# Kernel tuning notes

Hardware: AMD Instinct MI355X
Metric: run time of the kernel (lower is better)

## Reference

```python
import jax, jax.numpy as jnp
import numpy as np

B, T, U, H = 16, 256, 96, 512


def setup_inputs() -> dict:
    key = jax.random.key(0)
    k1, k2, k3, k4 = jax.random.split(key, 4)
    f = jax.random.normal(k1, (B, T, H), dtype=jnp.float32)
    g = jax.random.normal(k2, (B, U, H), dtype=jnp.float32)
    f_len = jax.random.randint(k3, (B,), 1, T + 1, dtype=jnp.int32)
    g_len = jax.random.randint(k4, (B,), 1, U + 1, dtype=jnp.int32)
    return {"f": f, "g": g, "f_len": f_len, "g_len": g_len}


def reference(f, g, f_len, g_len):
    # f: (B, T, H), g: (B, U, H) -> h: (B, T, U, H)
    # h[b,t,u,:] = f[b,t,:] + g[b,u,:] for t < f_len[b], u < g_len[b]; else 0.
    Bc, Tc, Hc = f.shape
    Uc = g.shape[1]
    t_valid = jnp.arange(Tc)[None, :] < f_len[:, None]          # (B, T)
    u_valid = jnp.arange(Uc)[None, :] < g_len[:, None]          # (B, U)
    mask = (t_valid[:, :, None] & u_valid[:, None, :])[..., None]  # (B, T, U, 1)
    h = f[:, :, None, :] + g[:, None, :, :]                     # (B, T, U, H)
    return jnp.where(mask, h, jnp.zeros((), dtype=f.dtype))
```

## Files before the change

### kernel.cpp

```cpp
#include <hip/hip_runtime.h>
#include <hip/hip_bf16.h>


#define TJ_B 16
#define TJ_T 256
#define TJ_U 96
#define TJ_H 512
#define TJ_H4 (TJ_H / 4)

typedef float fx4 __attribute__((ext_vector_type(4)));

__global__ __launch_bounds__(256) void TransducerJoint_66915590472509_kernel(
    const fx4* __restrict__ f,
    const fx4* __restrict__ g,
    const int* __restrict__ f_len,
    const int* __restrict__ g_len,
    fx4* __restrict__ out)
{
    const int bt = blockIdx.x;
    const int b  = bt >> 8;
    const int t  = bt & 255;

    const int h4    = threadIdx.x & (TJ_H4 - 1);
    const int uhalf = threadIdx.x >> 7;

    const int flen = f_len[b];
    const int glen = g_len[b];
    const bool tvalid = (t < flen);

    fx4 fv = (fx4)0.f;
    if (tvalid) fv = f[(size_t)bt * TJ_H4 + h4];

    const fx4* gp = g + ((size_t)(b * TJ_U + uhalf)) * TJ_H4 + h4;
    fx4* op = out + ((size_t)bt * TJ_U + uhalf) * TJ_H4 + h4;

    #pragma unroll 8
    for (int u = uhalf; u < TJ_U; u += 2) {
        const fx4 gv = *gp;
        const bool ok = tvalid && (u < glen);
        fx4 r = ok ? (fv + gv) : (fx4)0.f;
        __builtin_nontemporal_store(r, op);
        gp += 2 * TJ_H4;
        op += 2 * TJ_H4;
    }
}

extern "C" void kernel_launch(void* const* d_in, const int* in_sizes, int n_in,
                              void* d_out, int out_size, void* d_ws, size_t ws_size,
                              hipStream_t stream) {
    const fx4* f     = (const fx4*)d_in[0];
    const fx4* g     = (const fx4*)d_in[1];
    const int* f_len = (const int*)d_in[2];
    const int* g_len = (const int*)d_in[3];
    fx4*       out   = (fx4*)d_out;

    const int nblocks = TJ_B * TJ_T;
    TransducerJoint_66915590472509_kernel<<<nblocks, 256, 0, stream>>>(
        f, g, f_len, g_len, out);
}
```

Measured before the change: 806.0 us.

## Process two time steps per block, keeping g slice in registers

Each block now handles two consecutive t values with 512 threads. Each thread loads its share of g[b] into 24 registers once and reuses it for both time steps, which halves g reads per output. The nontemporal stores are replaced with plain stores, and f is loaded unconditionally. The cost is more register pressure and half as many blocks.

```diff
diff --git a/kernel.cpp b/kernel.cpp
--- a/kernel.cpp
+++ b/kernel.cpp
@@ -5,43 +5,52 @@
 #define TJ_B 16
 #define TJ_T 256
 #define TJ_U 96
-#define TJ_H 512
-#define TJ_H4 (TJ_H / 4)
+#define TJ_H4 128
+#define TJ_TT 2
+#define TJ_NTH 512
+#define TJ_K ((TJ_U * TJ_H4) / TJ_NTH)
 
 typedef float fx4 __attribute__((ext_vector_type(4)));
 
-__global__ __launch_bounds__(256) void TransducerJoint_66915590472509_kernel(
+__global__ __launch_bounds__(TJ_NTH) void TransducerJoint_66915590472509_kernel(
     const fx4* __restrict__ f,
     const fx4* __restrict__ g,
     const int* __restrict__ f_len,
     const int* __restrict__ g_len,
     fx4* __restrict__ out)
 {
-    const int bt = blockIdx.x;
-    const int b  = bt >> 8;
-    const int t  = bt & 255;
-
-    const int h4    = threadIdx.x & (TJ_H4 - 1);
-    const int uhalf = threadIdx.x >> 7;
+    const int bid = blockIdx.x;
+    const int b   = bid >> 7;
+    const int t0  = (bid & 127) * TJ_TT;
+    const int i   = threadIdx.x;
+    const int h4  = i & (TJ_H4 - 1);
+    const int uu  = i >> 7;
 
     const int flen = f_len[b];
     const int glen = g_len[b];
-    const bool tvalid = (t < flen);
 
-    fx4 fv = (fx4)0.f;
-    if (tvalid) fv = f[(size_t)bt * TJ_H4 + h4];
+    fx4 fr[TJ_TT];
+    #pragma unroll
+    for (int tt = 0; tt < TJ_TT; ++tt)
+        fr[tt] = f[(size_t)(b * TJ_T + t0 + tt) * TJ_H4 + h4];
 
-    const fx4* gp = g + ((size_t)(b * TJ_U + uhalf)) * TJ_H4 + h4;
-    fx4* op = out + ((size_t)bt * TJ_U + uhalf) * TJ_H4 + h4;
+    fx4 gr[TJ_K];
+    const fx4* gb = g + (size_t)b * (TJ_U * TJ_H4);
+    #pragma unroll
+    for (int k = 0; k < TJ_K; ++k)
+        gr[k] = gb[i + TJ_NTH * k];
 
-    #pragma unroll 8
-    for (int u = uhalf; u < TJ_U; u += 2) {
-        const fx4 gv = *gp;
-        const bool ok = tvalid && (u < glen);
-        fx4 r = ok ? (fv + gv) : (fx4)0.f;
-        __builtin_nontemporal_store(r, op);
-        gp += 2 * TJ_H4;
-        op += 2 * TJ_H4;
+    #pragma unroll
+    for (int tt = 0; tt < TJ_TT; ++tt) {
+        const int t = t0 + tt;
+        const bool tok = (t < flen);
+        const fx4 fv = fr[tt];
+        fx4* op = out + (size_t)(b * TJ_T + t) * (TJ_U * TJ_H4) + i;
+        #pragma unroll
+        for (int k = 0; k < TJ_K; ++k) {
+            const bool ok = tok && ((uu + 4 * k) < glen);
+            op[TJ_NTH * k] = ok ? (fv + gr[k]) : (fx4)0.f;
+        }
     }
 }
 
@@ -54,7 +63,7 @@
     const int* g_len = (const int*)d_in[3];
     fx4*       out   = (fx4*)d_out;
 
-    const int nblocks = TJ_B * TJ_T;
-    TransducerJoint_66915590472509_kernel<<<nblocks, 256, 0, stream>>>(
+    const int nblocks = TJ_B * (TJ_T / TJ_TT);
+    TransducerJoint_66915590472509_kernel<<<nblocks, TJ_NTH, 0, stream>>>(
         f, g, f_len, g_len, out);
 }
```

After: 794.1 us. Within noise of the previous version (-1.5%).
